# Optimization experiments

Measured on AMD Instinct MI355X. Metric: run time of the kernel, lower is better.

## Reference

```python
import jax, jax.numpy as jnp
import numpy as np

B, S, H, L, HEADS, VOCAB, POS = 32, 240, 1024, 8, 16, 48, 240
D = H // HEADS


def setup_inputs() -> dict:
    key = jax.random.key(0)
    ks = jax.random.split(key, 20)
    p = lambda k, shape: jax.random.normal(k, shape, jnp.float32) * 0.02
    x = jax.random.normal(ks[0], (B, S, VOCAB), jnp.float32)
    lengths = jnp.sort(jax.random.randint(ks[1], (B,), 120, S + 1))[::-1]
    lengths = lengths.at[0].set(S)  # padded max length == S
    return {
        "x": x,
        "w_emb": p(ks[2], (VOCAB, H)),
        "p_emb": p(ks[3], (POS, H)),
        "Wq": p(ks[4], (L, H, H)), "bq": p(ks[5], (L, H)),
        "Wk": p(ks[6], (L, H, H)), "bk": p(ks[7], (L, H)),
        "Wv": p(ks[8], (L, H, H)), "bv": p(ks[9], (L, H)),
        "W1": p(ks[10], (L, H, H)), "b1": p(ks[11], (L, H)),
        "W2": p(ks[12], (L, H, H)), "b2": p(ks[13], (L, H)),
        "ln1_s": jnp.ones((L, H), jnp.float32), "ln1_b": jnp.zeros((L, H), jnp.float32),
        "ln2_s": jnp.ones((L, H), jnp.float32), "ln2_b": jnp.zeros((L, H), jnp.float32),
        "Wfc": p(ks[14], (H, 4)), "bfc": p(ks[15], (4,)),
        "lengths": lengths,
    }


def _ln(x, s, b):
    m = jnp.mean(x, -1, keepdims=True)
    v = jnp.mean((x - m) ** 2, -1, keepdims=True)
    return (x - m) / jnp.sqrt(v + 1e-5) * s + b


def reference(x, w_emb, p_emb, Wq, bq, Wk, bk, Wv, bv, W1, b1, W2, b2,
              ln1_s, ln1_b, ln2_s, ln2_b, Wfc, bfc, lengths):
    tokens = jnp.argmax(x, -1)                      # [B,S] argmax over feature dim (48)
    valid = jnp.arange(S)[None, :] < lengths[:, None]  # [B,S] query-row validity
    # pack/unpack zeros out embeddings at padded positions; pos-enc added everywhere
    z = w_emb[tokens] * valid[..., None].astype(jnp.float32) + p_emb[None, :S]
    causal = jnp.tril(jnp.ones((S, S), bool))
    scale = 1.0 / jnp.sqrt(jnp.float32(H))          # source divides by sqrt(hidden), not sqrt(d_head)
    for i in range(L):
        q = (z @ Wq[i] + bq[i]).reshape(B, S, HEADS, D)
        k = (z @ Wk[i] + bk[i]).reshape(B, S, HEADS, D)
        v = (z @ Wv[i] + bv[i]).reshape(B, S, HEADS, D)
        scores = jnp.einsum('bqhd,bkhd->bhqk', q, k) * scale
        scores = jnp.where(causal, scores, -jnp.inf)
        # softmax over causal keys; padded query rows are zeroed (torch NaN->0 path)
        atten = jax.nn.softmax(scores, -1) * valid[:, None, :, None].astype(jnp.float32)
        out = jnp.einsum('bhqk,bkhd->bqhd', atten, v).reshape(B, S, H)
        z1 = _ln(z + out, ln1_s[i], ln1_b[i])       # dropout off in eval
        ff = jax.nn.gelu(z1 @ W1[i] + b1[i], approximate=False) @ W2[i] + b2[i]
        z = _ln(z1 + ff, ln2_s[i], ln2_b[i])
    z2 = jnp.mean(z, axis=1)                        # mean-pool includes padded positions (faithful)
    return jax.nn.softmax(z2 @ Wfc + bfc, axis=-1)
```

## Files before the change

kernel.cpp:

```cpp
#include <hip/hip_runtime.h>
#include <hip/hip_bf16.h>

#define Bz 32
#define Sz 240
#define Hz 1024
#define Lz 8
#define NHEADS 16
#define NVOCAB 48
#define DHEAD 64
#define VT_STRIDE 264

typedef unsigned short u16;
typedef unsigned int u32;
typedef __attribute__((ext_vector_type(8))) short short8v;
typedef __attribute__((ext_vector_type(4))) float floatx4;

__device__ __forceinline__ int get_len(const int* __restrict__ L, int b) {
  return (L[1] == 0) ? L[2 * b] : L[b];
}
__device__ __forceinline__ u16 f2bf(float f) {
  u32 u = __float_as_uint(f);
  return (u16)((u + 0x7FFFu + ((u >> 16) & 1u)) >> 16);
}
__device__ __forceinline__ float bf2f(u16 s) {
  return __uint_as_float(((u32)s) << 16);
}
__device__ __forceinline__ void async_copy16(const u16* g, u16* l) {
  __builtin_amdgcn_global_load_lds(
      (const __attribute__((address_space(1))) u32*)g,
      (__attribute__((address_space(3))) u32*)l, 16, 0, 0);
}

__global__ __launch_bounds__(256) void embed_kernel(
    const float* __restrict__ x, const float* __restrict__ w_emb,
    const float* __restrict__ p_emb, const int* __restrict__ lengths,
    float* __restrict__ z, u16* __restrict__ z_bf) {
  int bs = blockIdx.x;
  int b = bs / Sz, s = bs % Sz;
  __shared__ int stok;
  if (threadIdx.x == 0) {
    const float* xr = x + (size_t)bs * NVOCAB;
    float best = xr[0]; int bi = 0;
    for (int j = 1; j < NVOCAB; ++j) {
      float v = xr[j];
      if (v > best) { best = v; bi = j; }
    }
    stok = bi;
  }
  __syncthreads();
  int tok = stok;
  float valid = (s < get_len(lengths, b)) ? 1.f : 0.f;
  const float* we = w_emb + (size_t)tok * Hz;
  const float* pe = p_emb + (size_t)s * Hz;
  size_t base = (size_t)bs * Hz;
  for (int h = threadIdx.x; h < Hz; h += blockDim.x) {
    float v = we[h] * valid + pe[h];
    z[base + h] = v;
    z_bf[base + h] = f2bf(v);
  }
}

__global__ __launch_bounds__(256) void bias_concat(
    const float* __restrict__ bq, const float* __restrict__ bk,
    const float* __restrict__ bv, float* __restrict__ dst) {
  int i = blockIdx.x * 256 + threadIdx.x;
  int l = i / 3072, c = i % 3072;
  float v = (c < 1024) ? bq[l * 1024 + c]
          : (c < 2048) ? bk[l * 1024 + c - 1024]
                       : bv[l * 1024 + c - 2048];
  dst[i] = v;
}

struct WconvArgs { const float* src[5]; u16* dst[5]; };
__global__ __launch_bounds__(256) void wconv5(WconvArgs a) {
  __shared__ u16 T[32][33];
  const float* W = a.src[blockIdx.z];
  u16* wt = a.dst[blockIdx.z];
  int bi = blockIdx.y, bj = blockIdx.x;
  int r = threadIdx.x >> 3, c4 = (threadIdx.x & 7) * 4;
  float4 w4 = *(const float4*)(W + (size_t)(bi * 32 + r) * Hz + bj * 32 + c4);
  T[r][c4 + 0] = f2bf(w4.x); T[r][c4 + 1] = f2bf(w4.y);
  T[r][c4 + 2] = f2bf(w4.z); T[r][c4 + 3] = f2bf(w4.w);
  __syncthreads();
  u32 lo = (u32)T[c4 + 0][r] | ((u32)T[c4 + 1][r] << 16);
  u32 hi = (u32)T[c4 + 2][r] | ((u32)T[c4 + 3][r] << 16);
  uint2 val; val.x = lo; val.y = hi;
  *(uint2*)(wt + (size_t)(bj * 32 + r) * Hz + bi * 32 + c4) = val;
}

template <bool OUTBF16, bool GELU>
__global__ __launch_bounds__(256) void gemm_mfma(
    const u16* __restrict__ A, const u16* __restrict__ Wt,
    const float* __restrict__ bias, void* __restrict__ Cv, int nco) {
  __shared__ u16 As[4096];
  __shared__ u16 Bs[4096];
  int tid = threadIdx.x;
  int xt = nco >> 7;
  int id = blockIdx.x;
  int per = xt << 3;
  int g = id / per;
  int rr = id - g * per;
  int ys = 60 - (g << 3); ys = ys > 8 ? 8 : ys;
  int row0 = ((g << 3) + rr % ys) * 128;
  int col0 = (rr / ys) * 128;

  int w = tid >> 6, lane = tid & 63;
  int l15 = lane & 15, lq = lane >> 4;
  int wr = w >> 1, wc = w & 1;
  floatx4 acc[4][4] = {};

  const u16* gA0 = A + (size_t)(row0 + 32 * w + l15) * 1024 + 8 * lq;
  const u16* gA1 = gA0 + 16 * 1024;
  const u16* gB0 = Wt + (size_t)(col0 + 32 * w + l15) * 1024 + 8 * lq;
  const u16* gB1 = gB0 + 16 * 1024;
  u16* lA0 = As + (2 * w) * 512;
  u16* lA1 = lA0 + 512;
  u16* lB0 = Bs + (2 * w) * 512;
  u16* lB1 = lB0 + 512;

  int afrag_off[4], bfrag_off[4];
#pragma unroll
  for (int i = 0; i < 4; ++i) {
    afrag_off[i] = (wr * 4 + i) * 512 + lq * 128 + l15 * 8;
    bfrag_off[i] = (wc * 4 + i) * 512 + lq * 128 + l15 * 8;
  }

  for (int k0 = 0; k0 < 1024; k0 += 32) {
    async_copy16(gA0 + k0, lA0);
    async_copy16(gA1 + k0, lA1);
    async_copy16(gB0 + k0, lB0);
    async_copy16(gB1 + k0, lB1);
    __syncthreads();
    short8v af[4], bf[4];
#pragma unroll
    for (int i = 0; i < 4; ++i) af[i] = *(const short8v*)(As + afrag_off[i]);
#pragma unroll
    for (int i = 0; i < 4; ++i) bf[i] = *(const short8v*)(Bs + bfrag_off[i]);
#pragma unroll
    for (int mi = 0; mi < 4; ++mi)
#pragma unroll
      for (int ni = 0; ni < 4; ++ni)
        acc[mi][ni] = __builtin_amdgcn_mfma_f32_16x16x32_bf16(
            af[mi], bf[ni], acc[mi][ni], 0, 0, 0);
    __syncthreads();
  }

  int rowbase = row0 + wr * 64, colbase = col0 + wc * 64;
#pragma unroll
  for (int ni = 0; ni < 4; ++ni) {
    int col = colbase + ni * 16 + l15;
    float bcol = bias[col];
#pragma unroll
    for (int mi = 0; mi < 4; ++mi) {
      int rtop = rowbase + mi * 16 + lq * 4;
#pragma unroll
      for (int reg = 0; reg < 4; ++reg) {
        float vv = acc[mi][ni][reg] + bcol;
        if (GELU) vv = 0.5f * vv * (1.f + erff(vv * 0.70710678118654752f));
        if (OUTBF16)
          ((u16*)Cv)[(size_t)(rtop + reg) * nco + col] = f2bf(vv);
        else
          ((float*)Cv)[(size_t)(rtop + reg) * nco + col] = vv;
      }
    }
  }
}

__global__ __launch_bounds__(256) void attention_kernel(
    const u16* __restrict__ qkv, const int* __restrict__ lengths,
    float* __restrict__ out) {
  const int LDQ = 3072;
  __shared__ u16 Vt[64 * VT_STRIDE];
  __shared__ u16 Pb[4][16 * 40];
  int hh = blockIdx.x & 1;
  int h = (blockIdx.x >> 1) & 15;
  int b = blockIdx.x >> 5;
  int tid = threadIdx.x;
  const size_t base = ((size_t)b * Sz) * LDQ + (size_t)h * DHEAD;
  const u16* qp = qkv + base;
  const u16* kp = qkv + base + 1024;
  const u16* vp = qkv + base + 2048;

  for (int idx = tid; idx < 256 * 16; idx += 256) {
    int key = idx >> 4, d4 = (idx & 15) * 4;
    uint2 vv;
    if (key < Sz) vv = *(const uint2*)(vp + (size_t)key * LDQ + d4);
    else { vv.x = 0u; vv.y = 0u; }
    Vt[(d4 + 0) * VT_STRIDE + key] = (u16)(vv.x & 0xFFFF);
    Vt[(d4 + 1) * VT_STRIDE + key] = (u16)(vv.x >> 16);
    Vt[(d4 + 2) * VT_STRIDE + key] = (u16)(vv.y & 0xFFFF);
    Vt[(d4 + 3) * VT_STRIDE + key] = (u16)(vv.y >> 16);
  }
  __syncthreads();

  int w = tid >> 6, lane = tid & 63;
  int qgroup = lane >> 4, qcol = lane & 15;
  int len_b = get_len(lengths, b);

  for (int qt = hh * 8 + w; qt < hh * 8 + 8 && qt < 15; qt += 4) {
    const u16* qrow = qp + (size_t)(qt * 16 + qcol) * LDQ;
    short8v aq0 = *(const short8v*)(qrow + qgroup * 8);
    short8v aq1 = *(const short8v*)(qrow + 32 + qgroup * 8);
    floatx4 o0 = {0.f, 0.f, 0.f, 0.f}, o1 = o0, o2 = o0, o3 = o0;
    float m_run[4] = {-1e30f, -1e30f, -1e30f, -1e30f};
    float l_run[4] = {0.f, 0.f, 0.f, 0.f};
    int nsteps = (qt + 2) >> 1;

    for (int st = 0; st < nsteps; ++st) {
      int t0 = 2 * st, t1 = 2 * st + 1;
      bool has1 = (t1 <= qt);
      floatx4 s0 = {0.f, 0.f, 0.f, 0.f};
      {
        const u16* kr = kp + (size_t)(t0 * 16 + qcol) * LDQ;
        short8v bk0 = *(const short8v*)(kr + qgroup * 8);
        short8v bk1 = *(const short8v*)(kr + 32 + qgroup * 8);
        s0 = __builtin_amdgcn_mfma_f32_16x16x32_bf16(aq0, bk0, s0, 0, 0, 0);
        s0 = __builtin_amdgcn_mfma_f32_16x16x32_bf16(aq1, bk1, s0, 0, 0, 0);
      }
      floatx4 s1 = {0.f, 0.f, 0.f, 0.f};
      if (has1) {
        const u16* kr = kp + (size_t)(t1 * 16 + qcol) * LDQ;
        short8v bk0 = *(const short8v*)(kr + qgroup * 8);
        short8v bk1 = *(const short8v*)(kr + 32 + qgroup * 8);
        s1 = __builtin_amdgcn_mfma_f32_16x16x32_bf16(aq0, bk0, s1, 0, 0, 0);
        s1 = __builtin_amdgcn_mfma_f32_16x16x32_bf16(aq1, bk1, s1, 0, 0, 0);
      }
      int kg0 = t0 * 16 + qcol, kg1 = t1 * 16 + qcol;
      float p0[4], p1[4];
#pragma unroll
      for (int rg = 0; rg < 4; ++rg) {
        int row_g = qt * 16 + qgroup * 4 + rg;
        float x0 = (kg0 <= row_g) ? s0[rg] * 0.03125f : -1e30f;
        float x1 = (has1 && kg1 <= row_g) ? s1[rg] * 0.03125f : -1e30f;
        float mx = fmaxf(x0, x1);
        mx = fmaxf(mx, __shfl_xor(mx, 1));
        mx = fmaxf(mx, __shfl_xor(mx, 2));
        mx = fmaxf(mx, __shfl_xor(mx, 4));
        mx = fmaxf(mx, __shfl_xor(mx, 8));
        float mnew = fmaxf(m_run[rg], mx);
        float alpha = __expf(m_run[rg] - mnew);
        float e0 = __expf(x0 - mnew);
        float e1 = __expf(x1 - mnew);
        float rs = e0 + e1;
        rs += __shfl_xor(rs, 1);
        rs += __shfl_xor(rs, 2);
        rs += __shfl_xor(rs, 4);
        rs += __shfl_xor(rs, 8);
        l_run[rg] = l_run[rg] * alpha + rs;
        m_run[rg] = mnew;
        o0[rg] *= alpha; o1[rg] *= alpha; o2[rg] *= alpha; o3[rg] *= alpha;
        p0[rg] = e0; p1[rg] = e1;
      }
#pragma unroll
      for (int rg = 0; rg < 4; ++rg) {
        int rl = qgroup * 4 + rg;
        Pb[w][rl * 40 + qcol] = f2bf(p0[rg]);
        Pb[w][rl * 40 + 16 + qcol] = f2bf(p1[rg]);
      }
      __asm__ volatile("s_waitcnt lgkmcnt(0)" ::: "memory");
      short8v pa = *(const short8v*)(&Pb[w][qcol * 40 + qgroup * 8]);
      int kb0 = st * 32 + qgroup * 8;
      short8v bv0 = *(const short8v*)(&Vt[(0 * 16 + qcol) * VT_STRIDE + kb0]);
      short8v bv1 = *(const short8v*)(&Vt[(1 * 16 + qcol) * VT_STRIDE + kb0]);
      short8v bv2 = *(const short8v*)(&Vt[(2 * 16 + qcol) * VT_STRIDE + kb0]);
      short8v bv3 = *(const short8v*)(&Vt[(3 * 16 + qcol) * VT_STRIDE + kb0]);
      o0 = __builtin_amdgcn_mfma_f32_16x16x32_bf16(pa, bv0, o0, 0, 0, 0);
      o1 = __builtin_amdgcn_mfma_f32_16x16x32_bf16(pa, bv1, o1, 0, 0, 0);
      o2 = __builtin_amdgcn_mfma_f32_16x16x32_bf16(pa, bv2, o2, 0, 0, 0);
      o3 = __builtin_amdgcn_mfma_f32_16x16x32_bf16(pa, bv3, o3, 0, 0, 0);
    }

#pragma unroll
    for (int rg = 0; rg < 4; ++rg) {
      int row_g = qt * 16 + qgroup * 4 + rg;
      float vmask = (row_g < len_b) ? (1.f / l_run[rg]) : 0.f;
      float* op = out + ((size_t)b * Sz + row_g) * Hz + (size_t)h * DHEAD + qcol;
      op[0]  = o0[rg] * vmask;
      op[16] = o1[rg] * vmask;
      op[32] = o2[rg] * vmask;
      op[48] = o3[rg] * vmask;
    }
  }
}

__global__ __launch_bounds__(256) void add_ln_kernel(
    float* __restrict__ z, u16* __restrict__ z_bf, const float* __restrict__ r,
    const float* __restrict__ gamma, const float* __restrict__ beta) {
  int bs = blockIdx.x, tid = threadIdx.x;
  size_t base = (size_t)bs * Hz;
  __shared__ float sred[256];
  float vals[4];
  float sum = 0.f;
#pragma unroll
  for (int j = 0; j < 4; ++j) {
    int hh = tid + j * 256;
    vals[j] = z[base + hh] + r[base + hh];
    sum += vals[j];
  }
  sred[tid] = sum; __syncthreads();
  for (int off = 128; off > 0; off >>= 1) {
    if (tid < off) sred[tid] += sred[tid + off];
    __syncthreads();
  }
  float mean = sred[0] * (1.f / Hz); __syncthreads();
  float sq = 0.f;
#pragma unroll
  for (int j = 0; j < 4; ++j) { float d = vals[j] - mean; sq += d * d; }
  sred[tid] = sq; __syncthreads();
  for (int off = 128; off > 0; off >>= 1) {
    if (tid < off) sred[tid] += sred[tid + off];
    __syncthreads();
  }
  float rstd = rsqrtf(sred[0] * (1.f / Hz) + 1e-5f);
#pragma unroll
  for (int j = 0; j < 4; ++j) {
    int hh = tid + j * 256;
    float v = (vals[j] - mean) * rstd * gamma[hh] + beta[hh];
    z[base + hh] = v;
    z_bf[base + hh] = f2bf(v);
  }
}

__global__ __launch_bounds__(256) void pool_kernel(
    const float* __restrict__ z, const float* __restrict__ Wfc,
    const float* __restrict__ bfc, float* __restrict__ out) {
  int b = blockIdx.x, tid = threadIdx.x;
  __shared__ float red[256][4];
  float acc[4] = {0.f, 0.f, 0.f, 0.f};
  for (int hh = tid; hh < Hz; hh += 256) {
    float s = 0.f;
    for (int sp = 0; sp < Sz; ++sp) s += z[((size_t)(b * Sz + sp)) * Hz + hh];
    float z2 = s * (1.f / Sz);
#pragma unroll
    for (int c = 0; c < 4; ++c) acc[c] += z2 * Wfc[hh * 4 + c];
  }
#pragma unroll
  for (int c = 0; c < 4; ++c) red[tid][c] = acc[c];
  __syncthreads();
  for (int off = 128; off > 0; off >>= 1) {
    if (tid < off)
#pragma unroll
      for (int c = 0; c < 4; ++c) red[tid][c] += red[tid + off][c];
    __syncthreads();
  }
  if (tid == 0) {
    float lg[4], m = -1e30f;
#pragma unroll
    for (int c = 0; c < 4; ++c) { lg[c] = red[0][c] + bfc[c]; m = fmaxf(m, lg[c]); }
    float s = 0.f;
#pragma unroll
    for (int c = 0; c < 4; ++c) { lg[c] = expf(lg[c] - m); s += lg[c]; }
    float inv = 1.f / s;
#pragma unroll
    for (int c = 0; c < 4; ++c) out[b * 4 + c] = lg[c] * inv;
  }
}

extern "C" void kernel_launch(void* const* d_in, const int* in_sizes, int n_in,
                              void* d_out, int out_size, void* d_ws, size_t ws_size,
                              hipStream_t stream) {
  const float* x     = (const float*)d_in[0];
  const float* w_emb = (const float*)d_in[1];
  const float* p_emb = (const float*)d_in[2];
  const float* Wq = (const float*)d_in[3];
  const float* bq = (const float*)d_in[4];
  const float* Wk = (const float*)d_in[5];
  const float* bk = (const float*)d_in[6];
  const float* Wv = (const float*)d_in[7];
  const float* bv = (const float*)d_in[8];
  const float* W1 = (const float*)d_in[9];
  const float* b1 = (const float*)d_in[10];
  const float* W2 = (const float*)d_in[11];
  const float* b2 = (const float*)d_in[12];
  const float* ln1s = (const float*)d_in[13];
  const float* ln1b = (const float*)d_in[14];
  const float* ln2s = (const float*)d_in[15];
  const float* ln2b = (const float*)d_in[16];
  const float* Wfc  = (const float*)d_in[17];
  const float* bfc  = (const float*)d_in[18];
  const int* lengths = (const int*)d_in[19];
  float* out = (float*)d_out;

  const size_t BSH = (size_t)Bz * Sz * Hz;
  float* z    = (float*)d_ws;
  float* ao   = z + BSH;
  u16* z_bf   = (u16*)(ao + BSH);
  u16* ffb    = z_bf + BSH;
  u16* qkv    = ffb + BSH;
  u16* wt     = qkv + 3 * BSH;
  float* bqkv = (float*)(wt + 5 * 1024 * 1024);
  float* bo_f = (float*)qkv;

  embed_kernel<<<Bz * Sz, 256, 0, stream>>>(x, w_emb, p_emb, lengths, z, z_bf);
  bias_concat<<<Lz * 3072 / 256, 256, 0, stream>>>(bq, bk, bv, bqkv);

  for (int i = 0; i < Lz; ++i) {
    size_t wo = (size_t)i * Hz * Hz, bo = (size_t)i * Hz;
    WconvArgs wa;
    wa.src[0] = Wq + wo; wa.src[1] = Wk + wo; wa.src[2] = Wv + wo;
    wa.src[3] = W1 + wo; wa.src[4] = W2 + wo;
    wa.dst[0] = wt;                     wa.dst[1] = wt + 1024 * 1024;
    wa.dst[2] = wt + 2 * 1024 * 1024;   wa.dst[3] = wt + 3 * 1024 * 1024;
    wa.dst[4] = wt + 4 * 1024 * 1024;
    wconv5<<<dim3(32, 32, 5), 256, 0, stream>>>(wa);

    gemm_mfma<true, false><<<60 * 24, 256, 0, stream>>>(
        z_bf, wt, bqkv + (size_t)i * 3072, qkv, 3072);
    attention_kernel<<<Bz * NHEADS * 2, 256, 0, stream>>>(qkv, lengths, ao);
    add_ln_kernel<<<Bz * Sz, 256, 0, stream>>>(z, z_bf, ao, ln1s + bo, ln1b + bo);
    gemm_mfma<true, true><<<60 * 8, 256, 0, stream>>>(
        z_bf, wt + 3 * 1024 * 1024, b1 + bo, ffb, 1024);
    gemm_mfma<false, false><<<60 * 8, 256, 0, stream>>>(
        ffb, wt + 4 * 1024 * 1024, b2 + bo, bo_f, 1024);
    add_ln_kernel<<<Bz * Sz, 256, 0, stream>>>(z, z_bf, bo_f, ln2s + bo, ln2b + bo);
  }
  pool_kernel<<<Bz, 256, 0, stream>>>(z, Wfc, bfc, out);
}
```

Measured before the change: 2.273 ms.

## Double-buffer GEMM LDS, fuse residual adds, vectorize layernorm, split pooling

The GEMM main loop now uses two LDS buffers and prefetches the next K tile while the current one is computed, which removes one barrier per iteration. The residual add moves into the attention epilogue and into the second FFN GEMM epilogue, so the layernorm kernel only reads one input, and it now uses float4 loads and stores. Pooling is split into a parallel reduction across 8×32 blocks followed by a small FC and softmax kernel. Together these cut memory traffic and the serial work in the tail, at the cost of doubling GEMM shared memory.

```diff
diff --git a/kernel.cpp b/kernel.cpp
--- a/kernel.cpp
+++ b/kernel.cpp
@@ -88,12 +88,13 @@
   *(uint2*)(wt + (size_t)(bj * 32 + r) * Hz + bi * 32 + c4) = val;
 }
 
-template <bool OUTBF16, bool GELU>
+template <bool OUTBF16, bool GELU, bool RESID>
 __global__ __launch_bounds__(256) void gemm_mfma(
     const u16* __restrict__ A, const u16* __restrict__ Wt,
-    const float* __restrict__ bias, void* __restrict__ Cv, int nco) {
-  __shared__ u16 As[4096];
-  __shared__ u16 Bs[4096];
+    const float* __restrict__ bias, const float* __restrict__ resid,
+    void* __restrict__ Cv, int nco) {
+  __shared__ u16 As[2][4096];
+  __shared__ u16 Bs[2][4096];
   int tid = threadIdx.x;
   int xt = nco >> 7;
   int id = blockIdx.x;
@@ -113,10 +114,7 @@
   const u16* gA1 = gA0 + 16 * 1024;
   const u16* gB0 = Wt + (size_t)(col0 + 32 * w + l15) * 1024 + 8 * lq;
   const u16* gB1 = gB0 + 16 * 1024;
-  u16* lA0 = As + (2 * w) * 512;
-  u16* lA1 = lA0 + 512;
-  u16* lB0 = Bs + (2 * w) * 512;
-  u16* lB1 = lB0 + 512;
+  int sbase = (2 * w) * 512;
 
   int afrag_off[4], bfrag_off[4];
 #pragma unroll
@@ -125,24 +123,33 @@
     bfrag_off[i] = (wc * 4 + i) * 512 + lq * 128 + l15 * 8;
   }
 
-  for (int k0 = 0; k0 < 1024; k0 += 32) {
-    async_copy16(gA0 + k0, lA0);
-    async_copy16(gA1 + k0, lA1);
-    async_copy16(gB0 + k0, lB0);
-    async_copy16(gB1 + k0, lB1);
+  async_copy16(gA0, &As[0][sbase]);
+  async_copy16(gA1, &As[0][sbase + 512]);
+  async_copy16(gB0, &Bs[0][sbase]);
+  async_copy16(gB1, &Bs[0][sbase + 512]);
+
+  for (int it = 0; it < 32; ++it) {
     __syncthreads();
+    int nxt = it + 1;
+    if (nxt < 32) {
+      int nb = nxt & 1, k0 = nxt * 32;
+      async_copy16(gA0 + k0, &As[nb][sbase]);
+      async_copy16(gA1 + k0, &As[nb][sbase + 512]);
+      async_copy16(gB0 + k0, &Bs[nb][sbase]);
+      async_copy16(gB1 + k0, &Bs[nb][sbase + 512]);
+    }
+    int cb = it & 1;
     short8v af[4], bf[4];
 #pragma unroll
-    for (int i = 0; i < 4; ++i) af[i] = *(const short8v*)(As + afrag_off[i]);
-#pragma unroll
-    for (int i = 0; i < 4; ++i) bf[i] = *(const short8v*)(Bs + bfrag_off[i]);
+    for (int i = 0; i < 4; ++i) af[i] = *(const short8v*)(&As[cb][afrag_off[i]]);
+#pragma unroll
+    for (int i = 0; i < 4; ++i) bf[i] = *(const short8v*)(&Bs[cb][bfrag_off[i]]);
 #pragma unroll
     for (int mi = 0; mi < 4; ++mi)
 #pragma unroll
       for (int ni = 0; ni < 4; ++ni)
         acc[mi][ni] = __builtin_amdgcn_mfma_f32_16x16x32_bf16(
             af[mi], bf[ni], acc[mi][ni], 0, 0, 0);
-    __syncthreads();
   }
 
   int rowbase = row0 + wr * 64, colbase = col0 + wc * 64;
@@ -156,6 +163,7 @@
 #pragma unroll
       for (int reg = 0; reg < 4; ++reg) {
         float vv = acc[mi][ni][reg] + bcol;
+        if (RESID) vv += resid[(size_t)(rtop + reg) * nco + col];
         if (GELU) vv = 0.5f * vv * (1.f + erff(vv * 0.70710678118654752f));
         if (OUTBF16)
           ((u16*)Cv)[(size_t)(rtop + reg) * nco + col] = f2bf(vv);
@@ -168,7 +176,7 @@
 
 __global__ __launch_bounds__(256) void attention_kernel(
     const u16* __restrict__ qkv, const int* __restrict__ lengths,
-    float* __restrict__ out) {
+    const float* __restrict__ zres, float* __restrict__ out) {
   const int LDQ = 3072;
   __shared__ u16 Vt[64 * VT_STRIDE];
   __shared__ u16 Pb[4][16 * 40];
@@ -274,11 +282,11 @@
     for (int rg = 0; rg < 4; ++rg) {
       int row_g = qt * 16 + qgroup * 4 + rg;
       float vmask = (row_g < len_b) ? (1.f / l_run[rg]) : 0.f;
-      float* op = out + ((size_t)b * Sz + row_g) * Hz + (size_t)h * DHEAD + qcol;
-      op[0]  = o0[rg] * vmask;
-      op[16] = o1[rg] * vmask;
-      op[32] = o2[rg] * vmask;
-      op[48] = o3[rg] * vmask;
+      size_t ob = ((size_t)b * Sz + row_g) * Hz + (size_t)h * DHEAD + qcol;
+      out[ob]      = zres[ob]      + o0[rg] * vmask;
+      out[ob + 16] = zres[ob + 16] + o1[rg] * vmask;
+      out[ob + 32] = zres[ob + 32] + o2[rg] * vmask;
+      out[ob + 48] = zres[ob + 48] + o3[rg] * vmask;
     }
   }
 }
@@ -289,48 +297,60 @@
   int bs = blockIdx.x, tid = threadIdx.x;
   size_t base = (size_t)bs * Hz;
   __shared__ float sred[256];
-  float vals[4];
-  float sum = 0.f;
-#pragma unroll
-  for (int j = 0; j < 4; ++j) {
-    int hh = tid + j * 256;
-    vals[j] = z[base + hh] + r[base + hh];
-    sum += vals[j];
-  }
+  float4 v4 = *(const float4*)(r + base + tid * 4);
+  float sum = v4.x + v4.y + v4.z + v4.w;
   sred[tid] = sum; __syncthreads();
   for (int off = 128; off > 0; off >>= 1) {
     if (tid < off) sred[tid] += sred[tid + off];
     __syncthreads();
   }
   float mean = sred[0] * (1.f / Hz); __syncthreads();
-  float sq = 0.f;
-#pragma unroll
-  for (int j = 0; j < 4; ++j) { float d = vals[j] - mean; sq += d * d; }
-  sred[tid] = sq; __syncthreads();
+  float dx = v4.x - mean, dy = v4.y - mean, dz = v4.z - mean, dw = v4.w - mean;
+  sred[tid] = dx * dx + dy * dy + dz * dz + dw * dw; __syncthreads();
   for (int off = 128; off > 0; off >>= 1) {
     if (tid < off) sred[tid] += sred[tid + off];
     __syncthreads();
   }
   float rstd = rsqrtf(sred[0] * (1.f / Hz) + 1e-5f);
-#pragma unroll
-  for (int j = 0; j < 4; ++j) {
-    int hh = tid + j * 256;
-    float v = (vals[j] - mean) * rstd * gamma[hh] + beta[hh];
-    z[base + hh] = v;
-    z_bf[base + hh] = f2bf(v);
-  }
-}
-
-__global__ __launch_bounds__(256) void pool_kernel(
-    const float* __restrict__ z, const float* __restrict__ Wfc,
+  float4 g4 = *(const float4*)(gamma + tid * 4);
+  float4 b4 = *(const float4*)(beta + tid * 4);
+  float4 o;
+  o.x = dx * rstd * g4.x + b4.x;
+  o.y = dy * rstd * g4.y + b4.y;
+  o.z = dz * rstd * g4.z + b4.z;
+  o.w = dw * rstd * g4.w + b4.w;
+  *(float4*)(z + base + tid * 4) = o;
+  uint2 pk;
+  pk.x = (u32)f2bf(o.x) | ((u32)f2bf(o.y) << 16);
+  pk.y = (u32)f2bf(o.z) | ((u32)f2bf(o.w) << 16);
+  *(uint2*)(z_bf + base + tid * 4) = pk;
+}
+
+__global__ __launch_bounds__(256) void pool1_kernel(
+    const float* __restrict__ z, float* __restrict__ pooled) {
+  int chunk = blockIdx.x, b = blockIdx.y, tid = threadIdx.x;
+  int h = chunk * 128 + (tid & 127);
+  int half = tid >> 7;
+  __shared__ float sred[256];
+  const float* zp = z + ((size_t)b * Sz + half * 120) * Hz + h;
+  float s = 0.f;
+  for (int i = 0; i < 120; ++i) s += zp[(size_t)i * Hz];
+  sred[tid] = s; __syncthreads();
+  if (tid < 128)
+    pooled[(size_t)b * Hz + chunk * 128 + tid] =
+        (sred[tid] + sred[tid + 128]) * (1.f / Sz);
+}
+
+__global__ __launch_bounds__(256) void pool2_kernel(
+    const float* __restrict__ pooled, const float* __restrict__ Wfc,
     const float* __restrict__ bfc, float* __restrict__ out) {
   int b = blockIdx.x, tid = threadIdx.x;
   __shared__ float red[256][4];
   float acc[4] = {0.f, 0.f, 0.f, 0.f};
-  for (int hh = tid; hh < Hz; hh += 256) {
-    float s = 0.f;
-    for (int sp = 0; sp < Sz; ++sp) s += z[((size_t)(b * Sz + sp)) * Hz + hh];
-    float z2 = s * (1.f / Sz);
+#pragma unroll
+  for (int j = 0; j < 4; ++j) {
+    int hh = tid * 4 + j;
+    float z2 = pooled[(size_t)b * Hz + hh];
 #pragma unroll
     for (int c = 0; c < 4; ++c) acc[c] += z2 * Wfc[hh * 4 + c];
   }
@@ -389,7 +409,7 @@
   u16* qkv    = ffb + BSH;
   u16* wt     = qkv + 3 * BSH;
   float* bqkv = (float*)(wt + 5 * 1024 * 1024);
-  float* bo_f = (float*)qkv;
+  float* pooled = bqkv + Lz * 3072;
 
   embed_kernel<<<Bz * Sz, 256, 0, stream>>>(x, w_emb, p_emb, lengths, z, z_bf);
   bias_concat<<<Lz * 3072 / 256, 256, 0, stream>>>(bq, bk, bv, bqkv);
@@ -404,15 +424,16 @@
     wa.dst[4] = wt + 4 * 1024 * 1024;
     wconv5<<<dim3(32, 32, 5), 256, 0, stream>>>(wa);
 
-    gemm_mfma<true, false><<<60 * 24, 256, 0, stream>>>(
-        z_bf, wt, bqkv + (size_t)i * 3072, qkv, 3072);
-    attention_kernel<<<Bz * NHEADS * 2, 256, 0, stream>>>(qkv, lengths, ao);
+    gemm_mfma<true, false, false><<<60 * 24, 256, 0, stream>>>(
+        z_bf, wt, bqkv + (size_t)i * 3072, nullptr, qkv, 3072);
+    attention_kernel<<<Bz * NHEADS * 2, 256, 0, stream>>>(qkv, lengths, z, ao);
     add_ln_kernel<<<Bz * Sz, 256, 0, stream>>>(z, z_bf, ao, ln1s + bo, ln1b + bo);
-    gemm_mfma<true, true><<<60 * 8, 256, 0, stream>>>(
-        z_bf, wt + 3 * 1024 * 1024, b1 + bo, ffb, 1024);
-    gemm_mfma<false, false><<<60 * 8, 256, 0, stream>>>(
-        ffb, wt + 4 * 1024 * 1024, b2 + bo, bo_f, 1024);
-    add_ln_kernel<<<Bz * Sz, 256, 0, stream>>>(z, z_bf, bo_f, ln2s + bo, ln2b + bo);
-  }
-  pool_kernel<<<Bz, 256, 0, stream>>>(z, Wfc, bfc, out);
-}
+    gemm_mfma<true, true, false><<<60 * 8, 256, 0, stream>>>(
+        z_bf, wt + 3 * 1024 * 1024, b1 + bo, nullptr, ffb, 1024);
+    gemm_mfma<false, false, true><<<60 * 8, 256, 0, stream>>>(
+        ffb, wt + 4 * 1024 * 1024, b2 + bo, z, ao, 1024);
+    add_ln_kernel<<<Bz * Sz, 256, 0, stream>>>(z, z_bf, ao, ln2s + bo, ln2b + bo);
+  }
+  pool1_kernel<<<dim3(8, Bz), 256, 0, stream>>>(z, pooled);
+  pool2_kernel<<<Bz, 256, 0, stream>>>(pooled, Wfc, bfc, out);
+}
```

Measured after the change: 2.239 ms. No clear change (-1.5%).
